# Kernel tuning notes

Measured on AMD Instinct MI355X. Metric: run time of the kernel, lower is better.

## Reference

```python
import jax, jax.numpy as jnp
import numpy as np

B, A, D, H = 256, 16, 768, 512
LN_EPS = 1e-5


def setup_inputs() -> dict:
    key = jax.random.key(0)
    ks = jax.random.split(key, 8)
    aspects = jax.random.normal(ks[0], (B, A, D), dtype=jnp.float32)
    aspect_mask = jnp.ones((B, A), dtype=bool)
    # relation_gate: Linear(2D->H), ReLU, Dropout(eval=id), Linear(H->1)
    # xavier_uniform with gain=0.1, bias=-2.0 (per the module's custom init)
    lim1 = 0.1 * np.sqrt(6.0 / (2 * D + H))
    lim2 = 0.1 * np.sqrt(6.0 / (H + 1))
    W_g1 = jax.random.uniform(ks[1], (2 * D, H), jnp.float32, -lim1, lim1)
    b_g1 = jnp.full((H,), -2.0, dtype=jnp.float32)
    w_g2 = jax.random.uniform(ks[2], (H,), jnp.float32, -lim2, lim2)
    b_g2 = jnp.asarray(-2.0, dtype=jnp.float32)
    # composition: Linear(2D->H), ReLU, Dropout(eval=id), Linear(H->D), default init scale
    sc1 = 1.0 / np.sqrt(2 * D)
    sc2 = 1.0 / np.sqrt(H)
    W_c1 = jax.random.uniform(ks[3], (2 * D, H), jnp.float32, -sc1, sc1)
    b_c1 = jax.random.uniform(ks[4], (H,), jnp.float32, -sc1, sc1)
    W_c2 = jax.random.uniform(ks[5], (H, D), jnp.float32, -sc2, sc2)
    b_c2 = jax.random.uniform(ks[6], (D,), jnp.float32, -sc2, sc2)
    ln_gamma = jnp.ones((D,), dtype=jnp.float32)
    ln_beta = jnp.zeros((D,), dtype=jnp.float32)
    return {
        "aspects": aspects, "aspect_mask": aspect_mask,
        "W_g1": W_g1, "b_g1": b_g1, "w_g2": w_g2, "b_g2": b_g2,
        "W_c1": W_c1, "b_c1": b_c1, "W_c2": W_c2, "b_c2": b_c2,
        "ln_gamma": ln_gamma, "ln_beta": ln_beta,
    }


def reference(aspects, aspect_mask, W_g1, b_g1, w_g2, b_g2,
              W_c1, b_c1, W_c2, b_c2, ln_gamma, ln_beta):
    b, a, d = aspects.shape
    # cat([x_i, x_j]) @ W == x_i @ W[:D] + x_j @ W[D:]  -> batch all (i,j) pairs at once
    Wg_i, Wg_j = W_g1[:d], W_g1[d:]
    gi = jnp.einsum('bad,dh->bah', aspects, Wg_i)   # [B,A,H]
    gj = jnp.einsum('bad,dh->bah', aspects, Wg_j)   # [B,A,H]
    hg = jax.nn.relu(gi[:, :, None, :] + gj[:, None, :, :] + b_g1)  # [B,A,A,H]
    gate = jax.nn.sigmoid(jnp.einsum('bijh,h->bij', hg, w_g2) + b_g2)  # [B,A,A]
    eye = jnp.eye(a, dtype=bool)
    gate = jnp.where(eye[None], 0.0, gate)  # i==j pair skipped; all_gates diag stays 0

    Wc_i, Wc_j = W_c1[:d], W_c1[d:]
    ci = jnp.einsum('bad,dh->bah', aspects, Wc_i)
    cj = jnp.einsum('bad,dh->bah', aspects, Wc_j)
    hc = jax.nn.relu(ci[:, :, None, :] + cj[:, None, :, :] + b_c1)  # [B,A,A,H]
    composed = jnp.einsum('bijh,hd->bijd', hc, W_c2) + b_c2          # [B,A,A,D]
    # gated sum over source aspects j (gate is 0 on diag, masking i==j)
    influence = jnp.einsum('bij,bijd->bid', gate, composed)
    final = aspects + influence
    # LayerNorm over last dim
    mu = jnp.mean(final, axis=-1, keepdims=True)
    var = jnp.mean(jnp.square(final - mu), axis=-1, keepdims=True)
    final = (final - mu) * jax.lax.rsqrt(var + LN_EPS) * ln_gamma + ln_beta
    final = final * aspect_mask[..., None].astype(final.dtype)
    return final, gate
```

## Files before the change

kernel.cpp:

```cpp
#include <hip/hip_runtime.h>
#include <stdint.h>
#include <stddef.h>

typedef __attribute__((ext_vector_type(8))) short bf16x8;
typedef __attribute__((ext_vector_type(4))) float f32x4;
typedef __attribute__((ext_vector_type(8))) unsigned short u16x8;

typedef __attribute__((address_space(1))) unsigned int as1_u32;
typedef __attribute__((address_space(3))) unsigned int as3_u32;

__device__ __forceinline__ unsigned short f2b(float f) {
  union { unsigned int u; float f; } v; v.f = f;
  unsigned int u = v.u;
  return (unsigned short)((u + 0x7FFFu + ((u >> 16) & 1u)) >> 16);
}
__device__ __forceinline__ float b2f(unsigned short s) {
  union { unsigned int u; float f; } v; v.u = ((unsigned int)s) << 16; return v.f;
}
__device__ __forceinline__ void gld16(const unsigned short* g, unsigned short* l) {
  __builtin_amdgcn_global_load_lds((const as1_u32*)(unsigned int*)(size_t)(const void*)g,
                                   (as3_u32*)(unsigned int*)l, 16, 0, 0);
}

#define LN_EPS 1e-5f
#define BB 256
#define AA 16
#define DD 768
#define HH 512

__global__ __launch_bounds__(256) void prep(const float* __restrict__ Wg1,
                                            const float* __restrict__ Wc1,
                                            const float* __restrict__ Wc2,
                                            const float* __restrict__ aspects,
                                            unsigned short* __restrict__ Wt,
                                            unsigned short* __restrict__ Wc2t,
                                            unsigned short* __restrict__ Abf) {
  const int seg = blockIdx.z;
  if (seg == 5) {
    const int id = (blockIdx.y * 24 + blockIdx.x) * 256 + threadIdx.x + threadIdx.y * 32;
    for (int g = id; g < 393216; g += 147456) {
      const size_t i = (size_t)g * 8;
      const float4 f0 = *(const float4*)(aspects + i);
      const float4 f1 = *(const float4*)(aspects + i + 4);
      u16x8 p;
      p[0] = f2b(f0.x); p[1] = f2b(f0.y); p[2] = f2b(f0.z); p[3] = f2b(f0.w);
      p[4] = f2b(f1.x); p[5] = f2b(f1.y); p[6] = f2b(f1.z); p[7] = f2b(f1.w);
      *(u16x8*)(Abf + i) = p;
    }
    return;
  }
  const float* src;
  unsigned short* dst;
  int R, C;
  if (seg < 4) {
    src = (seg < 2 ? Wg1 : Wc1) + (size_t)(seg & 1) * DD * HH;
    dst = Wt + (size_t)seg * HH * DD;
    R = DD; C = HH;
  } else {
    src = Wc2; dst = Wc2t; R = HH; C = DD;
  }
  const int c0 = blockIdx.x * 32, r0 = blockIdx.y * 32;
  if (c0 >= C || r0 >= R) return;
  __shared__ float t[32][33];
  const int x = threadIdx.x;
  for (int yy = threadIdx.y; yy < 32; yy += 8)
    t[yy][x] = src[(size_t)(r0 + yy) * C + (c0 + x)];
  __syncthreads();
  for (int yy = threadIdx.y; yy < 32; yy += 8)
    dst[(size_t)(c0 + yy) * R + (r0 + x)] = f2b(t[x][yy]);
}

__global__ __launch_bounds__(256) void gemm1(const unsigned short* __restrict__ A,
                                             const unsigned short* __restrict__ Bt,
                                             unsigned short* __restrict__ P) {
  const int bx = blockIdx.x;
  const int mb = bx & 31, nb = bx >> 5;
  const int tid = threadIdx.x;
  const int w = tid >> 6, lane = tid & 63;
  const int lr = lane & 15, quad = lane >> 4;
  const int m0 = (w & 1) * 64, n0 = (w >> 1) * 32;
  const int K = DD;

  __shared__ __align__(16) unsigned short As[128 * 64];
  __shared__ __align__(16) unsigned short Bs[64 * 64];

  f32x4 acc[4][2] = {};

  const unsigned short* gsrc[6];
  unsigned short* lbase[6];
#pragma unroll
  for (int i = 0; i < 6; ++i) {
    const int cb = (i < 4) ? (w * 64 + i * 256) : (1024 + w * 64 + (i - 4) * 256);
    const int c = cb + lane;
    if (cb < 1024) {
      const int row = c >> 3, lcol = (c & 7) ^ (row & 7);
      gsrc[i]  = A + (size_t)(mb * 128 + row) * K + lcol * 8;
      lbase[i] = As + cb * 8;
    } else {
      const int p = c - 1024, row = p >> 3, lcol = (p & 7) ^ (row & 7);
      gsrc[i]  = Bt + (size_t)(nb * 64 + row) * K + lcol * 8;
      lbase[i] = Bs + (cb - 1024) * 8;
    }
  }

  for (int kk = 0; kk < K; kk += 64) {
    __syncthreads();
#pragma unroll
    for (int i = 0; i < 6; ++i) gld16(gsrc[i] + kk, lbase[i]);
    __syncthreads();
#pragma unroll
    for (int h = 0; h < 2; ++h) {
      bf16x8 a4[4], b2[2];
#pragma unroll
      for (int i = 0; i < 4; ++i) {
        const int row = m0 + i * 16 + lr;
        a4[i] = *(const bf16x8*)(As + row * 64 + (((quad + h * 4) ^ (row & 7)) * 8));
      }
#pragma unroll
      for (int j = 0; j < 2; ++j) {
        const int row = n0 + j * 16 + lr;
        b2[j] = *(const bf16x8*)(Bs + row * 64 + (((quad + h * 4) ^ (row & 7)) * 8));
      }
#pragma unroll
      for (int i = 0; i < 4; ++i)
#pragma unroll
        for (int j = 0; j < 2; ++j)
          acc[i][j] = __builtin_amdgcn_mfma_f32_16x16x32_bf16(a4[i], b2[j], acc[i][j], 0, 0, 0);
    }
  }

  const int rowb = mb * 128 + m0 + quad * 4;
  const int colb = nb * 64 + n0 + lr;
#pragma unroll
  for (int i = 0; i < 4; ++i)
#pragma unroll
    for (int j = 0; j < 2; ++j)
#pragma unroll
      for (int r = 0; r < 4; ++r)
        P[(size_t)(rowb + i * 16 + r) * 2048 + colb + j * 16] = f2b(acc[i][j][r]);
}

__global__ __launch_bounds__(1024) void pair1(
    const unsigned short* __restrict__ P,
    const float* __restrict__ bg1, const float* __restrict__ wg2,
    const float* __restrict__ bg2p, const float* __restrict__ bc1,
    unsigned short* __restrict__ u, float* __restrict__ gsum,
    float* __restrict__ gateO) {
  const int b = blockIdx.x;
  const int tid = threadIdx.x;
  const int v = tid >> 6;
  const int lane = tid & 63;

  __shared__ __align__(16) unsigned short S2[16 * 1024];

  const unsigned short* Pb = P + (size_t)b * 16 * 2048;
#pragma unroll
  for (int it = 0; it < 2; ++it) {
    const int c = tid + it * 1024;
    const int j = c >> 7, sub = c & 127;
    const unsigned short* src = Pb + (size_t)j * 2048 +
        (sub < 64 ? 512 + sub * 8 : 1536 + (sub - 64) * 8);
    gld16(src, S2 + c * 8);
  }

  float giR[8], ciR[8];
  {
    const u16x8 g8 = *(const u16x8*)(Pb + (size_t)v * 2048 + lane * 8);
    const u16x8 c8 = *(const u16x8*)(Pb + (size_t)v * 2048 + 1024 + lane * 8);
#pragma unroll
    for (int q = 0; q < 8; ++q) { giR[q] = b2f(g8[q]); ciR[q] = b2f(c8[q]); }
  }

  float bg1v[8], wg2v[8], bc1v[8];
  {
    const int h0 = lane * 8;
    const float4 a0 = *(const float4*)(bg1 + h0), a1 = *(const float4*)(bg1 + h0 + 4);
    const float4 b0 = *(const float4*)(wg2 + h0), b1 = *(const float4*)(wg2 + h0 + 4);
    const float4 c0 = *(const float4*)(bc1 + h0), c1 = *(const float4*)(bc1 + h0 + 4);
    bg1v[0] = a0.x; bg1v[1] = a0.y; bg1v[2] = a0.z; bg1v[3] = a0.w;
    bg1v[4] = a1.x; bg1v[5] = a1.y; bg1v[6] = a1.z; bg1v[7] = a1.w;
    wg2v[0] = b0.x; wg2v[1] = b0.y; wg2v[2] = b0.z; wg2v[3] = b0.w;
    wg2v[4] = b1.x; wg2v[5] = b1.y; wg2v[6] = b1.z; wg2v[7] = b1.w;
    bc1v[0] = c0.x; bc1v[1] = c0.y; bc1v[2] = c0.z; bc1v[3] = c0.w;
    bc1v[4] = c1.x; bc1v[5] = c1.y; bc1v[6] = c1.z; bc1v[7] = c1.w;
  }
  const float bg2s = bg2p[0];
  __syncthreads();

  float uac[8] = {0.f, 0.f, 0.f, 0.f, 0.f, 0.f, 0.f, 0.f};
  float gs = 0.f;
  for (int j0 = 0; j0 < 16; j0 += 2) {
    const u16x8 gj8a = *(const u16x8*)(S2 + (size_t)j0 * 1024 + lane * 8);
    const u16x8 cj8a = *(const u16x8*)(S2 + (size_t)j0 * 1024 + 512 + lane * 8);
    const u16x8 gj8b = *(const u16x8*)(S2 + (size_t)(j0 + 1) * 1024 + lane * 8);
    const u16x8 cj8b = *(const u16x8*)(S2 + (size_t)(j0 + 1) * 1024 + 512 + lane * 8);
    float dotA = 0.f, dotB = 0.f;
#pragma unroll
    for (int q = 0; q < 8; ++q) {
      dotA = fmaf(fmaxf(giR[q] + b2f(gj8a[q]) + bg1v[q], 0.f), wg2v[q], dotA);
      dotB = fmaf(fmaxf(giR[q] + b2f(gj8b[q]) + bg1v[q], 0.f), wg2v[q], dotB);
    }
#pragma unroll
    for (int off = 32; off; off >>= 1) {
      dotA += __shfl_xor(dotA, off);
      dotB += __shfl_xor(dotB, off);
    }
    const float gateA = (j0 == v)     ? 0.f : (1.f / (1.f + __expf(-(dotA + bg2s))));
    const float gateB = (j0 + 1 == v) ? 0.f : (1.f / (1.f + __expf(-(dotB + bg2s))));
    if (lane == 0) {
      gateO[((size_t)b * 16 + v) * 16 + j0] = gateA;
      gateO[((size_t)b * 16 + v) * 16 + j0 + 1] = gateB;
    }
    gs += gateA;
    gs += gateB;
#pragma unroll
    for (int q = 0; q < 8; ++q) {
      uac[q] = fmaf(gateA, fmaxf(ciR[q] + b2f(cj8a[q]) + bc1v[q], 0.f), uac[q]);
      uac[q] = fmaf(gateB, fmaxf(ciR[q] + b2f(cj8b[q]) + bc1v[q], 0.f), uac[q]);
    }
  }
  {
    u16x8 pk;
#pragma unroll
    for (int q = 0; q < 8; ++q) pk[q] = f2b(uac[q]);
    *(u16x8*)(u + (size_t)(b * 16 + v) * HH + lane * 8) = pk;
    if (lane == 0) gsum[b * 16 + v] = gs;
  }
}

__global__ __launch_bounds__(256) void gemm2(const unsigned short* __restrict__ u,
                                             const unsigned short* __restrict__ Wc2t,
                                             const float* __restrict__ gsum,
                                             const float* __restrict__ aspects,
                                             const float* __restrict__ bc2,
                                             float* __restrict__ outF) {
  const int mt = blockIdx.x & 31, nt = blockIdx.x >> 5;
  const int tid = threadIdx.x;
  const int w = tid >> 6, lane = tid & 63;
  const int lr = lane & 15, quad = lane >> 4;
  const int m0 = (w & 1) * 64, n0 = (w >> 1) * 48;

  __shared__ __align__(16) unsigned short As[128 * 64];
  __shared__ __align__(16) unsigned short Bs[96 * 64];

  f32x4 acc[4][3] = {};

  const unsigned short* gsrc[7];
  unsigned short* lbase[7];
#pragma unroll
  for (int i = 0; i < 7; ++i) {
    const int cb = w * 64 + i * 256;
    const int c = cb + lane;
    if (cb < 1024) {
      const int row = c >> 3, lcol = (c & 7) ^ (row & 7);
      gsrc[i]  = u + (size_t)(mt * 128 + row) * HH + lcol * 8;
      lbase[i] = As + cb * 8;
    } else {
      const int p = c - 1024, row = p >> 3, lcol = (p & 7) ^ (row & 7);
      gsrc[i]  = Wc2t + (size_t)(nt * 96 + row) * HH + lcol * 8;
      lbase[i] = Bs + (cb - 1024) * 8;
    }
  }

  for (int kk = 0; kk < HH; kk += 64) {
    __syncthreads();
#pragma unroll
    for (int i = 0; i < 7; ++i) gld16(gsrc[i] + kk, lbase[i]);
    __syncthreads();
#pragma unroll
    for (int h = 0; h < 2; ++h) {
      bf16x8 a4[4], b3[3];
#pragma unroll
      for (int i = 0; i < 4; ++i) {
        const int row = m0 + i * 16 + lr;
        a4[i] = *(const bf16x8*)(As + row * 64 + (((quad + h * 4) ^ (row & 7)) * 8));
      }
#pragma unroll
      for (int j = 0; j < 3; ++j) {
        const int row = n0 + j * 16 + lr;
        b3[j] = *(const bf16x8*)(Bs + row * 64 + (((quad + h * 4) ^ (row & 7)) * 8));
      }
#pragma unroll
      for (int i = 0; i < 4; ++i)
#pragma unroll
        for (int j = 0; j < 3; ++j)
          acc[i][j] = __builtin_amdgcn_mfma_f32_16x16x32_bf16(a4[i], b3[j], acc[i][j], 0, 0, 0);
    }
  }

#pragma unroll
  for (int i = 0; i < 4; ++i) {
#pragma unroll
    for (int r = 0; r < 4; ++r) {
      const int rowg = mt * 128 + m0 + i * 16 + quad * 4 + r;
      const float gsv = gsum[rowg];
#pragma unroll
      for (int j = 0; j < 3; ++j) {
        const int colg = nt * 96 + n0 + j * 16 + lr;
        outF[(size_t)rowg * DD + colg] =
            acc[i][j][r] + gsv * bc2[colg] + aspects[(size_t)rowg * DD + colg];
      }
    }
  }
}

__global__ __launch_bounds__(512) void lnfin(const float* __restrict__ gma,
                                             const float* __restrict__ bta,
                                             float* __restrict__ outF) {
  const int v = threadIdx.x >> 6, lane = threadIdx.x & 63;
  const int row = blockIdx.x * 8 + v;
  float* rp = outF + (size_t)row * DD;
  float4 x[3];
  float s1 = 0.f, s2 = 0.f;
#pragma unroll
  for (int s = 0; s < 3; ++s) {
    x[s] = *(const float4*)(rp + s * 256 + lane * 4);
    s1 += x[s].x + x[s].y + x[s].z + x[s].w;
    s2 += x[s].x * x[s].x + x[s].y * x[s].y + x[s].z * x[s].z + x[s].w * x[s].w;
  }
#pragma unroll
  for (int off = 32; off; off >>= 1) {
    s1 += __shfl_xor(s1, off);
    s2 += __shfl_xor(s2, off);
  }
  const float mu = s1 * (1.f / 768.f);
  const float var = s2 * (1.f / 768.f) - mu * mu;
  const float rs = rsqrtf(var + LN_EPS);
#pragma unroll
  for (int s = 0; s < 3; ++s) {
    const float4 g = *(const float4*)(gma + s * 256 + lane * 4);
    const float4 be = *(const float4*)(bta + s * 256 + lane * 4);
    float4 o;
    o.x = (x[s].x - mu) * rs * g.x + be.x;
    o.y = (x[s].y - mu) * rs * g.y + be.y;
    o.z = (x[s].z - mu) * rs * g.z + be.z;
    o.w = (x[s].w - mu) * rs * g.w + be.w;
    *(float4*)(rp + s * 256 + lane * 4) = o;
  }
}

extern "C" void kernel_launch(void* const* d_in, const int* in_sizes, int n_in,
                              void* d_out, int out_size, void* d_ws, size_t ws_size,
                              hipStream_t stream) {
  const float* aspects = (const float*)d_in[0];
  const float* W_g1 = (const float*)d_in[2];
  const float* b_g1 = (const float*)d_in[3];
  const float* w_g2 = (const float*)d_in[4];
  const float* b_g2 = (const float*)d_in[5];
  const float* W_c1 = (const float*)d_in[6];
  const float* b_c1 = (const float*)d_in[7];
  const float* W_c2 = (const float*)d_in[8];
  const float* b_c2 = (const float*)d_in[9];
  const float* ln_g = (const float*)d_in[10];
  const float* ln_b = (const float*)d_in[11];

  float* outF  = (float*)d_out;
  float* gateO = outF + (size_t)BB * AA * DD;

  char* ws = (char*)d_ws;
  unsigned short* Wt   = (unsigned short*)ws;
  unsigned short* Wc2t = (unsigned short*)(ws + 3145728);
  unsigned short* Abf  = (unsigned short*)(ws + 3932160);
  unsigned short* P    = (unsigned short*)(ws + 10223616);
  unsigned short* u    = (unsigned short*)(ws + 27000832);
  float* gsum          = (float*)(ws + 31195136);

  prep<<<dim3(24, 24, 6), dim3(32, 8, 1), 0, stream>>>(W_g1, W_c1, W_c2, aspects,
                                                       Wt, Wc2t, Abf);
  gemm1<<<1024, 256, 0, stream>>>(Abf, Wt, P);
  pair1<<<BB, 1024, 0, stream>>>(P, b_g1, w_g2, b_g2, b_c1, u, gsum, gateO);
  gemm2<<<256, 256, 0, stream>>>(u, Wc2t, gsum, aspects, b_c2, outF);
  lnfin<<<512, 512, 0, stream>>>(ln_g, ln_b, outF);
}
```

Measured before the change: 142.0 us.

## Double-buffer gemm1 LDS loads, widen N tile to 128, stage vectorized output

gemm1 now uses a 128x128 output tile per block (512 blocks instead of 1024), giving each wave a 4x4 MFMA accumulator grid. LDS is double-buffered so the next K-slice's global_load_lds is issued before the current slice is computed, with one barrier per iteration. The epilogue writes bf16 results into padded LDS and then stores 16-byte vectors to P instead of scattered 2-byte stores. In exchange it uses more registers and 64KB of LDS, which may reduce occupancy, and there are half as many blocks to spread across the CUs.

```diff
diff --git a/kernel.cpp b/kernel.cpp
--- a/kernel.cpp
+++ b/kernel.cpp
@@ -78,66 +78,88 @@
   const int tid = threadIdx.x;
   const int w = tid >> 6, lane = tid & 63;
   const int lr = lane & 15, quad = lane >> 4;
-  const int m0 = (w & 1) * 64, n0 = (w >> 1) * 32;
+  const int m0 = (w & 1) * 64, n0 = (w >> 1) * 64;
   const int K = DD;
 
-  __shared__ __align__(16) unsigned short As[128 * 64];
-  __shared__ __align__(16) unsigned short Bs[64 * 64];
-
-  f32x4 acc[4][2] = {};
-
-  const unsigned short* gsrc[6];
-  unsigned short* lbase[6];
-#pragma unroll
-  for (int i = 0; i < 6; ++i) {
-    const int cb = (i < 4) ? (w * 64 + i * 256) : (1024 + w * 64 + (i - 4) * 256);
+  __shared__ __align__(16) unsigned short Ls[2][16384];
+
+  f32x4 acc[4][4] = {};
+
+  const unsigned short* gsrc[8];
+  int loff[8];
+#pragma unroll
+  for (int i = 0; i < 8; ++i) {
+    const int cb = w * 64 + i * 256;
     const int c = cb + lane;
     if (cb < 1024) {
       const int row = c >> 3, lcol = (c & 7) ^ (row & 7);
-      gsrc[i]  = A + (size_t)(mb * 128 + row) * K + lcol * 8;
-      lbase[i] = As + cb * 8;
+      gsrc[i] = A + (size_t)(mb * 128 + row) * K + lcol * 8;
+      loff[i] = cb * 8;
     } else {
       const int p = c - 1024, row = p >> 3, lcol = (p & 7) ^ (row & 7);
-      gsrc[i]  = Bt + (size_t)(nb * 64 + row) * K + lcol * 8;
-      lbase[i] = Bs + (cb - 1024) * 8;
-    }
-  }
-
+      gsrc[i] = Bt + (size_t)(nb * 128 + row) * K + lcol * 8;
+      loff[i] = (cb - 1024) * 8 + 8192;
+    }
+  }
+
+#pragma unroll
+  for (int i = 0; i < 8; ++i) gld16(gsrc[i], Ls[0] + loff[i]);
+  asm volatile("s_waitcnt vmcnt(0)" ::: "memory");
+  __builtin_amdgcn_s_barrier();
+
+  int cur = 0;
   for (int kk = 0; kk < K; kk += 64) {
-    __syncthreads();
-#pragma unroll
-    for (int i = 0; i < 6; ++i) gld16(gsrc[i] + kk, lbase[i]);
-    __syncthreads();
+    if (kk + 64 < K) {
+#pragma unroll
+      for (int i = 0; i < 8; ++i) gld16(gsrc[i] + kk + 64, Ls[cur ^ 1] + loff[i]);
+    }
+    const unsigned short* As = Ls[cur];
+    const unsigned short* Bs = Ls[cur] + 8192;
 #pragma unroll
     for (int h = 0; h < 2; ++h) {
-      bf16x8 a4[4], b2[2];
+      bf16x8 a4[4], b4[4];
 #pragma unroll
       for (int i = 0; i < 4; ++i) {
         const int row = m0 + i * 16 + lr;
         a4[i] = *(const bf16x8*)(As + row * 64 + (((quad + h * 4) ^ (row & 7)) * 8));
       }
 #pragma unroll
-      for (int j = 0; j < 2; ++j) {
+      for (int j = 0; j < 4; ++j) {
         const int row = n0 + j * 16 + lr;
-        b2[j] = *(const bf16x8*)(Bs + row * 64 + (((quad + h * 4) ^ (row & 7)) * 8));
+        b4[j] = *(const bf16x8*)(Bs + row * 64 + (((quad + h * 4) ^ (row & 7)) * 8));
       }
 #pragma unroll
       for (int i = 0; i < 4; ++i)
 #pragma unroll
-        for (int j = 0; j < 2; ++j)
-          acc[i][j] = __builtin_amdgcn_mfma_f32_16x16x32_bf16(a4[i], b2[j], acc[i][j], 0, 0, 0);
-    }
-  }
-
-  const int rowb = mb * 128 + m0 + quad * 4;
-  const int colb = nb * 64 + n0 + lr;
+        for (int j = 0; j < 4; ++j)
+          acc[i][j] = __builtin_amdgcn_mfma_f32_16x16x32_bf16(a4[i], b4[j], acc[i][j], 0, 0, 0);
+    }
+    asm volatile("s_waitcnt lgkmcnt(0)" ::: "memory");
+    asm volatile("s_waitcnt vmcnt(0)" ::: "memory");
+    __builtin_amdgcn_s_barrier();
+    cur ^= 1;
+  }
+
+  __syncthreads();
+  unsigned short* CS = (unsigned short*)Ls;
 #pragma unroll
   for (int i = 0; i < 4; ++i)
 #pragma unroll
-    for (int j = 0; j < 2; ++j)
-#pragma unroll
-      for (int r = 0; r < 4; ++r)
-        P[(size_t)(rowb + i * 16 + r) * 2048 + colb + j * 16] = f2b(acc[i][j][r]);
+    for (int j = 0; j < 4; ++j)
+#pragma unroll
+      for (int r = 0; r < 4; ++r) {
+        const int rl = m0 + i * 16 + quad * 4 + r;
+        const int cl = n0 + j * 16 + lr;
+        CS[rl * 132 + cl] = f2b(acc[i][j][r]);
+      }
+  __syncthreads();
+  const int c8 = (tid & 15) * 8;
+#pragma unroll
+  for (int p = 0; p < 8; ++p) {
+    const int row = p * 16 + (tid >> 4);
+    const u16x8 v = *(const u16x8*)(CS + row * 132 + c8);
+    *(u16x8*)(P + (size_t)(mb * 128 + row) * 2048 + nb * 128 + c8) = v;
+  }
 }
 
 __global__ __launch_bounds__(1024) void pair1(
@@ -367,7 +389,7 @@
 
   prep<<<dim3(24, 24, 6), dim3(32, 8, 1), 0, stream>>>(W_g1, W_c1, W_c2, aspects,
                                                        Wt, Wc2t, Abf);
-  gemm1<<<1024, 256, 0, stream>>>(Abf, Wt, P);
+  gemm1<<<512, 256, 0, stream>>>(Abf, Wt, P);
   pair1<<<BB, 1024, 0, stream>>>(P, b_g1, w_g2, b_g2, b_c1, u, gsum, gateO);
   gemm2<<<256, 256, 0, stream>>>(u, Wc2t, gsum, aspects, b_c2, outF);
   lnfin<<<512, 512, 0, stream>>>(ln_g, ln_b, outF);
```

Result: no change. 141.5 us (-0.3%).
